# Kernel tuning notes

Hardware: AMD Instinct MI355X
Metric: run time of the kernel (lower is better)

Reference implementation:

```python
import jax, jax.numpy as jnp
import numpy as np

TAU = 0.1
K = 60.0
CHUNK = 64
B = 1024


def setup_inputs() -> dict:
    key = jax.random.key(0)
    k1, k2, k3, k4, k5, k6 = jax.random.split(key, 6)
    s_v = jax.random.normal(k1, (B, B), dtype=jnp.float32)
    s_l = jax.random.normal(k2, (B, B), dtype=jnp.float32)
    pos_mask = jax.random.randint(k3, (B, B), 0, 2).astype(jnp.bool_)
    neg_mask = jax.random.randint(k4, (B, B), 0, 2).astype(jnp.bool_)
    w_v = jax.random.uniform(k5, (B, B), dtype=jnp.float32)
    w_l = jax.random.uniform(k6, (B, B), dtype=jnp.float32)
    return {"s_v": s_v, "s_l": s_l, "pos_mask": pos_mask,
            "neg_mask": neg_mask, "w_v": w_v, "w_l": w_l}


def _soft_ranks(sim, pos_f, neg_f, tau):
    """Chunked differentiable soft ranks. sim/pos_f/neg_f: [B, B] float."""
    b = sim.shape[0]
    n_chunks = b // CHUNK
    sim_c = sim.reshape(n_chunks, CHUNK, b)
    pos_c = pos_f.reshape(n_chunks, CHUNK, b)
    neg_c = neg_f.reshape(n_chunks, CHUNK, b)

    def per_chunk(args):
        cs, pf, nf = args  # each [CHUNK, B]
        # diff[c, a, b] = s[c, a] - s[c, b]
        sig = jax.nn.sigmoid((cs[:, :, None] - cs[:, None, :]) / tau)  # [CHUNK, B, B]
        rank_pos = 1.0 + jnp.einsum('cab,ca->cb', sig, nf)  # count negatives above
        rank_neg = 1.0 + jnp.einsum('cab,ca->cb', sig, pf)  # count positives above
        return rank_pos * pf + rank_neg * nf

    ranks = jax.lax.map(per_chunk, (sim_c, pos_c, neg_c))  # [n_chunks, CHUNK, B]
    return ranks.reshape(b, b)


def reference(s_v, s_l, pos_mask, neg_mask, w_v, w_l):
    pos_f = pos_mask.astype(s_v.dtype)
    neg_f = neg_mask.astype(s_v.dtype)
    rank_v = _soft_ranks(s_v, pos_f, neg_f, TAU)
    rank_l = _soft_ranks(s_l, pos_f, neg_f, TAU)
    S_hat = (K + 1.0) * (w_v / (K + rank_v) + w_l / (K + rank_l))
    return S_hat
```

## Files before the change

kernel.cpp:

```cpp
#include <hip/hip_runtime.h>
#include <hip/hip_fp16.h>

constexpr int B = 1024;
constexpr int NT = 256;
constexpr int NB = 60;
constexpr int SLOTCAP = 1216;
constexpr int QCAP = SLOTCAP / 4;
constexpr int QPHYS = QCAP + (QCAP >> 4) + 1;
constexpr float L2E = 1.4426950408889634f;
constexpr int TCOLS = NB + 6;

constexpr int OFF_EN  = 0;
constexpr int OFF_CQ  = OFF_EN + SLOTCAP * 4;
constexpr int OFF_SEG = OFF_CQ + 2 * QPHYS * 16;
constexpr int OFF_BKQ = OFF_SEG + 14 * TCOLS * 4;
constexpr int OFF_SST = OFF_BKQ + QCAP;
constexpr int OFF_RED = OFF_SST + (NB + 1) * 4;
constexpr int POOL_BYTES = ((OFF_RED + 32 + 15) / 16) * 16;

__global__ __launch_bounds__(NT, 8)
void rank_one_kernel(const float* __restrict__ s_v, const float* __restrict__ s_l,
                     const int* __restrict__ pos_m, const int* __restrict__ neg_m,
                     float* __restrict__ rank_ws) {
    __shared__ __align__(16) char pool[POOL_BYTES];
    float* En          = (float*)(pool + OFF_EN);
    float4* CeAll      = (float4*)(pool + OFF_CQ);
    uint4* ChAll       = (uint4*)(pool + OFF_CQ + QPHYS*16);
    unsigned char (*segCnt)[16]  = (unsigned char(*)[16])(pool + OFF_SEG);
    unsigned short (*segPre)[16] = (unsigned short(*)[16])(pool + OFF_SEG + NB*16);
    float* TabF        = (float*)(pool + OFF_SEG);
    int* segStart      = (int*)(pool + OFF_SST);
    float* Red         = (float*)(pool + OFF_RED);
    float* ANnode      = (float*)(pool + OFF_CQ);
    float* APnode      = ANnode + 64;

    const int m = blockIdx.x >> 10;
    const int r = blockIdx.x & 1023;
    const float* __restrict__ S = m ? s_l : s_v;
    const int tid = threadIdx.x;
    const int lane = tid & 63;
    const int wvid = tid >> 6;
    const unsigned long long lmask = (1ull << lane) - 1ull;

    for (int s = tid; s < SLOTCAP; s += NT) En[s] = 0.f;
    for (int j = tid; j < NB * 16 / 4; j += NT) ((int*)segCnt)[j] = 0;
    __syncthreads();

    float uu[4]; int cat[4];
    float mn = 1e30f, mx = -1e30f;
#pragma unroll
    for (int i = 0; i < 4; ++i) {
        const int c = tid + i * NT;
        uu[i] = S[r * B + c] * 10.0f;
        const int pf = pos_m[r * B + c] != 0, nf = neg_m[r * B + c] != 0;
        cat[i] = pf | (nf << 1);
        mn = fminf(mn, uu[i]); mx = fmaxf(mx, uu[i]);
    }
#pragma unroll
    for (int off = 1; off < 64; off <<= 1) {
        mn = fminf(mn, __shfl_xor(mn, off));
        mx = fmaxf(mx, __shfl_xor(mx, off));
    }
    if (lane == 0) { Red[wvid] = mn; Red[4 + wvid] = mx; }
    __syncthreads();

    const float lo = fminf(fminf(Red[0], Red[1]), fminf(Red[2], Red[3]));
    const float hi = fmaxf(fmaxf(Red[4], Red[5]), fmaxf(Red[6], Red[7]));
    const float umin = lo;
    const float Wb   = fmaxf((hi - lo) * (1.0001f / NB), 1.0f);
    const float invW = 1.0f / Wb;
    const float kap1 = exp2f(-Wb * L2E);
    const float kap2 = kap1 * kap1;
    const float kap3 = kap2 * kap1;
    const float eWm  = exp2f(Wb * L2E);

    int key[4], rk[4];
#pragma unroll
    for (int i = 0; i < 4; ++i) {
        int b = (int)((uu[i] - umin) * invW);
        b = b > NB - 1 ? NB - 1 : b;
        const int kk = cat[i] ? b : 63;
        key[i] = b;
        unsigned long long same = ~0ull;
#pragma unroll
        for (int j = 0; j < 6; ++j) {
            const unsigned long long bb = __ballot((kk >> j) & 1);
            same &= ((kk >> j) & 1) ? bb : ~bb;
        }
        rk[i] = (int)__popcll(same & lmask);
        if (cat[i] && rk[i] == 0)
            segCnt[kk][i * 4 + wvid] = (unsigned char)__popcll(same);
    }
    __syncthreads();

    for (int j = tid; j < NB * 16; j += NT) {
        const int k = j >> 4, u = j & 15;
        int p = 0;
        for (int v = 0; v < u; ++v) p += (int)segCnt[k][v];
        segPre[k][u] = (unsigned short)p;
    }
    if (wvid == 0) {
        int t = 0;
        if (lane < NB) {
#pragma unroll
            for (int u = 0; u < 16; ++u) t += (int)segCnt[lane][u];
            t = (t + 3) & ~3;
        }
        int inc = t;
#pragma unroll
        for (int d = 1; d < 64; d <<= 1) {
            const int o = __shfl_up(inc, d);
            if (lane >= d) inc += o;
        }
        if (lane < NB) segStart[lane] = inc - t;
        if (lane == NB - 1) segStart[NB] = inc;
    }
    __syncthreads();

#pragma unroll
    for (int i = 0; i < 4; ++i) {
        if (cat[i]) {
            const int k = key[i];
            const int slot = segStart[k] + (int)segPre[k][i * 4 + wvid] + rk[i];
            const float cb = umin + ((float)k + 0.5f) * Wb;
            const float env = exp2f((uu[i] - cb) * L2E);
            unsigned eb = __float_as_uint(env);
            eb = (eb & ~3u) | (unsigned)cat[i];
            En[slot] = __uint_as_float(eb);
        }
    }
    __syncthreads();

    const int nS = segStart[NB];
    const int nQ = nS >> 2;

    if (tid < 14 * 6) {
        const int row = tid / 6, ci = tid % 6;
        TabF[row * TCOLS + (ci < 2 ? ci : ci + 60)] = 0.f;
    }
    for (int q = tid; q < nQ; q += NT) {
        const float4 e4v = *(const float4*)&En[4 * q];
        const float en[4] = {e4v.x, e4v.y, e4v.z, e4v.w};
        const int fl[4] = {(int)(__float_as_uint(e4v.x) & 3u),
                           (int)(__float_as_uint(e4v.y) & 3u),
                           (int)(__float_as_uint(e4v.z) & 3u),
                           (int)(__float_as_uint(e4v.w) & 3u)};
        const float s01 = en[0] + en[1], p01 = en[0] * en[1];
        const float s23 = en[2] + en[3], p23 = en[2] * en[3];
        const float e1 = s01 + s23;
        const float e2 = fmaf(s01, s23, p01 + p23);
        const float e3 = fmaf(s01, p23, s23 * p01);
        const float e4 = p01 * p23;
        float nA3 = 0.f, nA2 = 0.f, nA1 = 0.f, nA0 = 0.f;
        float nP3 = 0.f, nP2 = 0.f, nP1 = 0.f, nP0 = 0.f;
#pragma unroll
        for (int j = 0; j < 4; ++j) {
            const float b1 = e1 - en[j];
            const float b2 = fmaf(-en[j], b1, e2);
            const float b3 = fmaf(-en[j], b2, e3);
            const float nn = (float)(fl[j] >> 1) * en[j];
            const float pp = (float)(fl[j] & 1) * en[j];
            nA3 += nn; nA2 = fmaf(nn, b1, nA2); nA1 = fmaf(nn, b2, nA1); nA0 = fmaf(nn, b3, nA0);
            nP3 += pp; nP2 = fmaf(pp, b1, nP2); nP1 = fmaf(pp, b2, nP1); nP0 = fmaf(pp, b3, nP0);
        }
        const int pq = q + (q >> 4);
        CeAll[pq] = make_float4(e1, e2, e3, e4);
        __half2 hA0 = __floats2half2_rn(nA3, nA2);
        __half2 hA1 = __floats2half2_rn(nA1, nA0);
        __half2 hP0 = __floats2half2_rn(nP3, nP2);
        __half2 hP1 = __floats2half2_rn(nP1, nP0);
        ChAll[pq] = make_uint4(reinterpret_cast<unsigned&>(hA0), reinterpret_cast<unsigned&>(hA1),
                               reinterpret_cast<unsigned&>(hP0), reinterpret_cast<unsigned&>(hP1));
    }
    if (tid < NB * 4) {
        const int k = tid >> 2, o = tid & 3;
        float g1a=0,g2a=0,g3a=0,h1a=0,h2a=0,h3a=0,s0a=0;
        float g1p=0,g2p=0,g3p=0,h1p=0,h2p=0,h3p=0,s0p=0;
        for (int s = segStart[k] + o; s < segStart[k + 1]; s += 4) {
            const float en = En[s];
            const int f = (int)(__float_as_uint(en) & 3u);
            if (!f) continue;
            const float en2 = en * en, en3 = en2 * en;
            const float ren = __builtin_amdgcn_rcpf(en);
            const float ren2 = ren * ren, ren3 = ren2 * ren;
            const float nf = (float)(f >> 1), pf = (float)(f & 1);
            g1a = fmaf(nf,en,g1a);  g2a = fmaf(nf,en2,g2a);  g3a = fmaf(nf,en3,g3a);
            h1a = fmaf(nf,ren,h1a); h2a = fmaf(nf,ren2,h2a); h3a = fmaf(nf,ren3,h3a); s0a += nf;
            g1p = fmaf(pf,en,g1p);  g2p = fmaf(pf,en2,g2p);  g3p = fmaf(pf,en3,g3p);
            h1p = fmaf(pf,ren,h1p); h2p = fmaf(pf,ren2,h2p); h3p = fmaf(pf,ren3,h3p); s0p += pf;
        }
#define RED4(v) v += __shfl_xor(v, 2); v += __shfl_xor(v, 1)
        RED4(g1a); RED4(g2a); RED4(g3a); RED4(h1a); RED4(h2a); RED4(h3a); RED4(s0a);
        RED4(g1p); RED4(g2p); RED4(g3p); RED4(h1p); RED4(h2p); RED4(h3p); RED4(s0p);
#undef RED4
        if (o == 0) {
            TabF[(0*7+0)*TCOLS+k+2]=g1a; TabF[(0*7+1)*TCOLS+k+2]=g2a; TabF[(0*7+2)*TCOLS+k+2]=g3a;
            TabF[(0*7+3)*TCOLS+k+2]=h1a; TabF[(0*7+4)*TCOLS+k+2]=h2a; TabF[(0*7+5)*TCOLS+k+2]=h3a;
            TabF[(0*7+6)*TCOLS+k+2]=s0a;
            TabF[(1*7+0)*TCOLS+k+2]=g1p; TabF[(1*7+1)*TCOLS+k+2]=g2p; TabF[(1*7+2)*TCOLS+k+2]=g3p;
            TabF[(1*7+3)*TCOLS+k+2]=h1p; TabF[(1*7+4)*TCOLS+k+2]=h2p; TabF[(1*7+5)*TCOLS+k+2]=h3p;
            TabF[(1*7+6)*TCOLS+k+2]=s0p;
        }
    }
    __syncthreads();
    for (int rowi = wvid; rowi < 14; rowi += 4) {
        const int r7 = rowi % 7;
        float* Trow = &TabF[rowi * TCOLS];
        float v = (lane < NB) ? Trow[lane + 2] : 0.f;
        if (r7 < 3) {
            float kp = (r7 == 0) ? kap1 : (r7 == 1 ? kap2 : kap3);
#pragma unroll
            for (int d = 1; d < 64; d <<= 1) {
                const float o = __shfl_up(v, d);
                if (lane >= d) v = fmaf(kp, o, v);
                kp *= kp;
            }
        } else {
            float kp = (r7 == 3) ? kap1 : (r7 == 4 ? kap2 : (r7 == 5 ? kap3 : 1.0f));
#pragma unroll
            for (int d = 1; d < 64; d <<= 1) {
                float o = __shfl_down(v, d);
                if (lane + d > 63) o = 0.f;
                v = fmaf(kp, o, v);
                kp *= kp;
            }
        }
        if (lane < NB) Trow[lane + 2] = v;
    }
    __syncthreads();

    const int nd = tid >> 2;
    const int no = tid & 3;
    float ANv = 0.f, APv = 0.f;
    if (nd < NB) {
        const int klo = nd > 0 ? nd - 1 : 0;
        const int khi = nd < NB - 1 ? nd + 1 : NB - 1;
        const int qs  = segStart[klo] >> 2;
        const int qe  = segStart[khi + 1] >> 2;
        const int qo0 = segStart[nd] >> 2;
        const int qo1 = segStart[nd + 1] >> 2;
        for (int q = qs + no; q < qe; q += 4) {
            const float x = (q < qo0) ? eWm : ((q >= qo1) ? kap1 : 1.0f);
            const int pq = q + (q >> 4);
            const float4 ce = CeAll[pq];
            const uint4 ch = ChAll[pq];
            const float2 a01 = __half22float2(*(const __half2*)&ch.x);
            const float2 a23 = __half22float2(*(const __half2*)&ch.y);
            const float2 p01 = __half22float2(*(const __half2*)&ch.z);
            const float2 p23 = __half22float2(*(const __half2*)&ch.w);
            float t = x + ce.x; t = fmaf(t, x, ce.y); t = fmaf(t, x, ce.z);
            const float D = fmaf(t, x, ce.w);
            float u = fmaf(a01.x, x, a01.y); u = fmaf(u, x, a23.x);
            const float NA = fmaf(u, x, a23.y);
            float v = fmaf(p01.x, x, p01.y); v = fmaf(v, x, p23.x);
            const float NP = fmaf(v, x, p23.y);
            const float rd = __builtin_amdgcn_rcpf(D);
            ANv = fmaf(NA, rd, ANv);
            APv = fmaf(NP, rd, APv);
        }
        ANv += __shfl_xor(ANv, 2); ANv += __shfl_xor(ANv, 1);
        APv += __shfl_xor(APv, 2); APv += __shfl_xor(APv, 1);
        const float k2 = kap2, k4 = kap2 * kap2, k6 = k4 * kap2;
        ANv += k2 * TabF[(0*7+0)*TCOLS+nd] - k4 * TabF[(0*7+1)*TCOLS+nd] + k6 * TabF[(0*7+2)*TCOLS+nd]
             + TabF[(0*7+6)*TCOLS+nd+4] - k2 * TabF[(0*7+3)*TCOLS+nd+4]
             + k4 * TabF[(0*7+4)*TCOLS+nd+4] - k6 * TabF[(0*7+5)*TCOLS+nd+4];
        APv += k2 * TabF[(1*7+0)*TCOLS+nd] - k4 * TabF[(1*7+1)*TCOLS+nd] + k6 * TabF[(1*7+2)*TCOLS+nd]
             + TabF[(1*7+6)*TCOLS+nd+4] - k2 * TabF[(1*7+3)*TCOLS+nd+4]
             + k4 * TabF[(1*7+4)*TCOLS+nd+4] - k6 * TabF[(1*7+5)*TCOLS+nd+4];
    }
    __syncthreads();
    if (nd < NB && no == 0) { ANnode[nd] = ANv; APnode[nd] = APv; }
    __syncthreads();

#pragma unroll
    for (int i = 0; i < 4; ++i) {
        const float t = (uu[i] - umin) * invW - 0.5f;
        int jc = (int)floorf(t);
        jc = jc < 1 ? 1 : (jc > NB - 3 ? NB - 3 : jc);
        const float s = t - (float)jc;
        const float sm = s - 1.f, sp = s + 1.f, s2 = s - 2.f;
        const float wL = -s * sm * s2 * (1.f / 6.f);
        const float w0 = sp * sm * s2 * 0.5f;
        const float w1 = -sp * s * s2 * 0.5f;
        const float w2 = sp * s * sm * (1.f / 6.f);
        const float AN = wL * ANnode[jc-1] + w0 * ANnode[jc] + w1 * ANnode[jc+1] + w2 * ANnode[jc+2];
        const float AP = wL * APnode[jc-1] + w0 * APnode[jc] + w1 * APnode[jc+1] + w2 * APnode[jc+2];
        const bool pf = (cat[i] & 1) != 0;
        const bool nf = (cat[i] & 2) != 0;
        const float rk_ = (pf ? 1.f + AN : 0.f) + (nf ? 1.f + AP : 0.f);
        rank_ws[m * (B * B) + r * B + (tid + i * NT)] = rk_;
    }
}

__global__ __launch_bounds__(NT, 8)
void combine_kernel(const float* __restrict__ rank_ws,
                    const float* __restrict__ w_v, const float* __restrict__ w_l,
                    float* __restrict__ out) {
    const int i4 = (blockIdx.x * NT + threadIdx.x) * 4;
    const float4 rv = *(const float4*)&rank_ws[i4];
    const float4 rl = *(const float4*)&rank_ws[B * B + i4];
    const float4 wv = *(const float4*)&w_v[i4];
    const float4 wl = *(const float4*)&w_l[i4];
    float4 o;
    o.x = 61.f * (wv.x / (60.f + rv.x) + wl.x / (60.f + rl.x));
    o.y = 61.f * (wv.y / (60.f + rv.y) + wl.y / (60.f + rl.y));
    o.z = 61.f * (wv.z / (60.f + rv.z) + wl.z / (60.f + rl.z));
    o.w = 61.f * (wv.w / (60.f + rv.w) + wl.w / (60.f + rl.w));
    *(float4*)&out[i4] = o;
}

extern "C" void kernel_launch(void* const* d_in, const int* in_sizes, int n_in,
                              void* d_out, int out_size, void* d_ws, size_t ws_size,
                              hipStream_t stream) {
    const float* s_v = (const float*)d_in[0];
    const float* s_l = (const float*)d_in[1];
    const int* pos_mask = (const int*)d_in[2];
    const int* neg_mask = (const int*)d_in[3];
    const float* w_v = (const float*)d_in[4];
    const float* w_l = (const float*)d_in[5];
    float* out = (float*)d_out;
    float* rank_ws = (float*)d_ws;

    rank_one_kernel<<<2 * B, NT, 0, stream>>>(s_v, s_l, pos_mask, neg_mask, rank_ws);
    combine_kernel<<<(B * B) / (NT * 4), NT, 0, stream>>>(rank_ws, w_v, w_l, out);
}
```

Before: 31.21 us.

## Fuse both modality rank computations and combine step into one kernel per row

Each block now processes one row for both s_v and s_l in sequence, reusing the mask loads and shared-memory scratch, and writes the final combined output directly. This removes the 8 MB rank workspace round trip through global memory and the second kernel launch. In exchange the grid halves to 1024 blocks, each running the two passes serially, which reduces the parallelism available to hide latency.

```diff
diff --git a/kernel.cpp b/kernel.cpp
--- a/kernel.cpp
+++ b/kernel.cpp
@@ -13,15 +13,15 @@
 constexpr int OFF_EN  = 0;
 constexpr int OFF_CQ  = OFF_EN + SLOTCAP * 4;
 constexpr int OFF_SEG = OFF_CQ + 2 * QPHYS * 16;
-constexpr int OFF_BKQ = OFF_SEG + 14 * TCOLS * 4;
-constexpr int OFF_SST = OFF_BKQ + QCAP;
+constexpr int OFF_SST = OFF_SEG + 14 * TCOLS * 4;
 constexpr int OFF_RED = OFF_SST + (NB + 1) * 4;
-constexpr int POOL_BYTES = ((OFF_RED + 32 + 15) / 16) * 16;
+constexpr int POOL_BYTES = ((OFF_RED + 64 + 15) / 16) * 16;
 
 __global__ __launch_bounds__(NT, 8)
-void rank_one_kernel(const float* __restrict__ s_v, const float* __restrict__ s_l,
-                     const int* __restrict__ pos_m, const int* __restrict__ neg_m,
-                     float* __restrict__ rank_ws) {
+void rank_fused_kernel(const float* __restrict__ s_v, const float* __restrict__ s_l,
+                       const int* __restrict__ pos_m, const int* __restrict__ neg_m,
+                       const float* __restrict__ w_v, const float* __restrict__ w_l,
+                       float* __restrict__ out) {
     __shared__ __align__(16) char pool[POOL_BYTES];
     float* En          = (float*)(pool + OFF_EN);
     float4* CeAll      = (float4*)(pool + OFF_CQ);
@@ -34,279 +34,285 @@
     float* ANnode      = (float*)(pool + OFF_CQ);
     float* APnode      = ANnode + 64;
 
-    const int m = blockIdx.x >> 10;
-    const int r = blockIdx.x & 1023;
-    const float* __restrict__ S = m ? s_l : s_v;
+    const int r = blockIdx.x;
     const int tid = threadIdx.x;
     const int lane = tid & 63;
     const int wvid = tid >> 6;
     const unsigned long long lmask = (1ull << lane) - 1ull;
 
-    for (int s = tid; s < SLOTCAP; s += NT) En[s] = 0.f;
-    for (int j = tid; j < NB * 16 / 4; j += NT) ((int*)segCnt)[j] = 0;
-    __syncthreads();
-
-    float uu[4]; int cat[4];
-    float mn = 1e30f, mx = -1e30f;
+    float uu[2][4]; int cat[4];
+    float mn0 = 1e30f, mx0 = -1e30f, mn1 = 1e30f, mx1 = -1e30f;
 #pragma unroll
     for (int i = 0; i < 4; ++i) {
         const int c = tid + i * NT;
-        uu[i] = S[r * B + c] * 10.0f;
+        uu[0][i] = s_v[r * B + c] * 10.0f;
+        uu[1][i] = s_l[r * B + c] * 10.0f;
         const int pf = pos_m[r * B + c] != 0, nf = neg_m[r * B + c] != 0;
         cat[i] = pf | (nf << 1);
-        mn = fminf(mn, uu[i]); mx = fmaxf(mx, uu[i]);
+        mn0 = fminf(mn0, uu[0][i]); mx0 = fmaxf(mx0, uu[0][i]);
+        mn1 = fminf(mn1, uu[1][i]); mx1 = fmaxf(mx1, uu[1][i]);
     }
 #pragma unroll
     for (int off = 1; off < 64; off <<= 1) {
-        mn = fminf(mn, __shfl_xor(mn, off));
-        mx = fmaxf(mx, __shfl_xor(mx, off));
-    }
-    if (lane == 0) { Red[wvid] = mn; Red[4 + wvid] = mx; }
+        mn0 = fminf(mn0, __shfl_xor(mn0, off)); mx0 = fmaxf(mx0, __shfl_xor(mx0, off));
+        mn1 = fminf(mn1, __shfl_xor(mn1, off)); mx1 = fmaxf(mx1, __shfl_xor(mx1, off));
+    }
+    if (lane == 0) {
+        Red[0 + wvid] = mn0; Red[4 + wvid] = mx0;
+        Red[8 + wvid] = mn1; Red[12 + wvid] = mx1;
+    }
     __syncthreads();
 
-    const float lo = fminf(fminf(Red[0], Red[1]), fminf(Red[2], Red[3]));
-    const float hi = fmaxf(fmaxf(Red[4], Red[5]), fmaxf(Red[6], Red[7]));
-    const float umin = lo;
-    const float Wb   = fmaxf((hi - lo) * (1.0001f / NB), 1.0f);
-    const float invW = 1.0f / Wb;
-    const float kap1 = exp2f(-Wb * L2E);
-    const float kap2 = kap1 * kap1;
-    const float kap3 = kap2 * kap1;
-    const float eWm  = exp2f(Wb * L2E);
-
-    int key[4], rk[4];
+    float umin2[2], Wb2[2], invW2[2], kapA[2], kapB[2], kapC[2], eWm2[2];
+#pragma unroll
+    for (int mp = 0; mp < 2; ++mp) {
+        const float lo = fminf(fminf(Red[8*mp+0], Red[8*mp+1]), fminf(Red[8*mp+2], Red[8*mp+3]));
+        const float hi = fmaxf(fmaxf(Red[8*mp+4], Red[8*mp+5]), fmaxf(Red[8*mp+6], Red[8*mp+7]));
+        umin2[mp] = lo;
+        Wb2[mp]   = fmaxf((hi - lo) * (1.0001f / NB), 1.0f);
+        invW2[mp] = 1.0f / Wb2[mp];
+        kapA[mp]  = exp2f(-Wb2[mp] * L2E);
+        kapB[mp]  = kapA[mp] * kapA[mp];
+        kapC[mp]  = kapB[mp] * kapA[mp];
+        eWm2[mp]  = exp2f(Wb2[mp] * L2E);
+    }
+
+    float rkm[2][4];
+
+#pragma unroll
+    for (int mp = 0; mp < 2; ++mp) {
+        const float umin = umin2[mp], Wb = Wb2[mp], invW = invW2[mp];
+        const float kap1 = kapA[mp], kap2 = kapB[mp], kap3 = kapC[mp], eWm = eWm2[mp];
+
+        __syncthreads();
+        for (int s = tid; s < SLOTCAP; s += NT) En[s] = 0.f;
+        for (int j = tid; j < NB * 16 / 4; j += NT) ((int*)segCnt)[j] = 0;
+        __syncthreads();
+
+        int key[4], rk[4];
+#pragma unroll
+        for (int i = 0; i < 4; ++i) {
+            int b = (int)((uu[mp][i] - umin) * invW);
+            b = b > NB - 1 ? NB - 1 : b;
+            const int kk = cat[i] ? b : 63;
+            key[i] = b;
+            unsigned long long same = ~0ull;
+#pragma unroll
+            for (int j = 0; j < 6; ++j) {
+                const unsigned long long bb = __ballot((kk >> j) & 1);
+                same &= ((kk >> j) & 1) ? bb : ~bb;
+            }
+            rk[i] = (int)__popcll(same & lmask);
+            if (cat[i] && rk[i] == 0)
+                segCnt[kk][i * 4 + wvid] = (unsigned char)__popcll(same);
+        }
+        __syncthreads();
+
+        for (int j = tid; j < NB * 16; j += NT) {
+            const int k = j >> 4, u = j & 15;
+            int p = 0;
+            for (int v = 0; v < u; ++v) p += (int)segCnt[k][v];
+            segPre[k][u] = (unsigned short)p;
+        }
+        if (wvid == 0) {
+            int t = 0;
+            if (lane < NB) {
+#pragma unroll
+                for (int u = 0; u < 16; ++u) t += (int)segCnt[lane][u];
+                t = (t + 3) & ~3;
+            }
+            int inc = t;
+#pragma unroll
+            for (int d = 1; d < 64; d <<= 1) {
+                const int o = __shfl_up(inc, d);
+                if (lane >= d) inc += o;
+            }
+            if (lane < NB) segStart[lane] = inc - t;
+            if (lane == NB - 1) segStart[NB] = inc;
+        }
+        __syncthreads();
+
+#pragma unroll
+        for (int i = 0; i < 4; ++i) {
+            if (cat[i]) {
+                const int k = key[i];
+                const int slot = segStart[k] + (int)segPre[k][i * 4 + wvid] + rk[i];
+                const float cb = umin + ((float)k + 0.5f) * Wb;
+                const float env = exp2f((uu[mp][i] - cb) * L2E);
+                unsigned eb = __float_as_uint(env);
+                eb = (eb & ~3u) | (unsigned)cat[i];
+                En[slot] = __uint_as_float(eb);
+            }
+        }
+        __syncthreads();
+
+        const int nS = segStart[NB];
+        const int nQ = nS >> 2;
+
+        if (tid < 14 * 6) {
+            const int row = tid / 6, ci = tid % 6;
+            TabF[row * TCOLS + (ci < 2 ? ci : ci + 60)] = 0.f;
+        }
+        for (int q = tid; q < nQ; q += NT) {
+            const float4 e4v = *(const float4*)&En[4 * q];
+            const float en[4] = {e4v.x, e4v.y, e4v.z, e4v.w};
+            const int fl[4] = {(int)(__float_as_uint(e4v.x) & 3u),
+                               (int)(__float_as_uint(e4v.y) & 3u),
+                               (int)(__float_as_uint(e4v.z) & 3u),
+                               (int)(__float_as_uint(e4v.w) & 3u)};
+            const float s01 = en[0] + en[1], p01 = en[0] * en[1];
+            const float s23 = en[2] + en[3], p23 = en[2] * en[3];
+            const float e1 = s01 + s23;
+            const float e2 = fmaf(s01, s23, p01 + p23);
+            const float e3 = fmaf(s01, p23, s23 * p01);
+            const float e4 = p01 * p23;
+            float nA3 = 0.f, nA2 = 0.f, nA1 = 0.f, nA0 = 0.f;
+            float nP3 = 0.f, nP2 = 0.f, nP1 = 0.f, nP0 = 0.f;
+#pragma unroll
+            for (int j = 0; j < 4; ++j) {
+                const float b1 = e1 - en[j];
+                const float b2 = fmaf(-en[j], b1, e2);
+                const float b3 = fmaf(-en[j], b2, e3);
+                const float nn = (float)(fl[j] >> 1) * en[j];
+                const float pp = (float)(fl[j] & 1) * en[j];
+                nA3 += nn; nA2 = fmaf(nn, b1, nA2); nA1 = fmaf(nn, b2, nA1); nA0 = fmaf(nn, b3, nA0);
+                nP3 += pp; nP2 = fmaf(pp, b1, nP2); nP1 = fmaf(pp, b2, nP1); nP0 = fmaf(pp, b3, nP0);
+            }
+            const int pq = q + (q >> 4);
+            CeAll[pq] = make_float4(e1, e2, e3, e4);
+            __half2 hA0 = __floats2half2_rn(nA3, nA2);
+            __half2 hA1 = __floats2half2_rn(nA1, nA0);
+            __half2 hP0 = __floats2half2_rn(nP3, nP2);
+            __half2 hP1 = __floats2half2_rn(nP1, nP0);
+            ChAll[pq] = make_uint4(reinterpret_cast<unsigned&>(hA0), reinterpret_cast<unsigned&>(hA1),
+                                   reinterpret_cast<unsigned&>(hP0), reinterpret_cast<unsigned&>(hP1));
+        }
+        if (tid < NB * 4) {
+            const int k = tid >> 2, o = tid & 3;
+            float g1a=0,g2a=0,g3a=0,h1a=0,h2a=0,h3a=0,s0a=0;
+            float g1p=0,g2p=0,g3p=0,h1p=0,h2p=0,h3p=0,s0p=0;
+            for (int s = segStart[k] + o; s < segStart[k + 1]; s += 4) {
+                const float en = En[s];
+                const int f = (int)(__float_as_uint(en) & 3u);
+                if (!f) continue;
+                const float en2 = en * en, en3 = en2 * en;
+                const float ren = __builtin_amdgcn_rcpf(en);
+                const float ren2 = ren * ren, ren3 = ren2 * ren;
+                const float nf = (float)(f >> 1), pf = (float)(f & 1);
+                g1a = fmaf(nf,en,g1a);  g2a = fmaf(nf,en2,g2a);  g3a = fmaf(nf,en3,g3a);
+                h1a = fmaf(nf,ren,h1a); h2a = fmaf(nf,ren2,h2a); h3a = fmaf(nf,ren3,h3a); s0a += nf;
+                g1p = fmaf(pf,en,g1p);  g2p = fmaf(pf,en2,g2p);  g3p = fmaf(pf,en3,g3p);
+                h1p = fmaf(pf,ren,h1p); h2p = fmaf(pf,ren2,h2p); h3p = fmaf(pf,ren3,h3p); s0p += pf;
+            }
+#define RED4(v) v += __shfl_xor(v, 2); v += __shfl_xor(v, 1)
+            RED4(g1a); RED4(g2a); RED4(g3a); RED4(h1a); RED4(h2a); RED4(h3a); RED4(s0a);
+            RED4(g1p); RED4(g2p); RED4(g3p); RED4(h1p); RED4(h2p); RED4(h3p); RED4(s0p);
+#undef RED4
+            if (o == 0) {
+                TabF[(0*7+0)*TCOLS+k+2]=g1a; TabF[(0*7+1)*TCOLS+k+2]=g2a; TabF[(0*7+2)*TCOLS+k+2]=g3a;
+                TabF[(0*7+3)*TCOLS+k+2]=h1a; TabF[(0*7+4)*TCOLS+k+2]=h2a; TabF[(0*7+5)*TCOLS+k+2]=h3a;
+                TabF[(0*7+6)*TCOLS+k+2]=s0a;
+                TabF[(1*7+0)*TCOLS+k+2]=g1p; TabF[(1*7+1)*TCOLS+k+2]=g2p; TabF[(1*7+2)*TCOLS+k+2]=g3p;
+                TabF[(1*7+3)*TCOLS+k+2]=h1p; TabF[(1*7+4)*TCOLS+k+2]=h2p; TabF[(1*7+5)*TCOLS+k+2]=h3p;
+                TabF[(1*7+6)*TCOLS+k+2]=s0p;
+            }
+        }
+        __syncthreads();
+        for (int rowi = wvid; rowi < 14; rowi += 4) {
+            const int r7 = rowi % 7;
+            float* Trow = &TabF[rowi * TCOLS];
+            float v = (lane < NB) ? Trow[lane + 2] : 0.f;
+            if (r7 < 3) {
+                float kp = (r7 == 0) ? kap1 : (r7 == 1 ? kap2 : kap3);
+#pragma unroll
+                for (int d = 1; d < 64; d <<= 1) {
+                    const float o = __shfl_up(v, d);
+                    if (lane >= d) v = fmaf(kp, o, v);
+                    kp *= kp;
+                }
+            } else {
+                float kp = (r7 == 3) ? kap1 : (r7 == 4 ? kap2 : (r7 == 5 ? kap3 : 1.0f));
+#pragma unroll
+                for (int d = 1; d < 64; d <<= 1) {
+                    float o = __shfl_down(v, d);
+                    if (lane + d > 63) o = 0.f;
+                    v = fmaf(kp, o, v);
+                    kp *= kp;
+                }
+            }
+            if (lane < NB) Trow[lane + 2] = v;
+        }
+        __syncthreads();
+
+        const int nd = tid >> 2;
+        const int no = tid & 3;
+        float ANv = 0.f, APv = 0.f;
+        if (nd < NB) {
+            const int klo = nd > 0 ? nd - 1 : 0;
+            const int khi = nd < NB - 1 ? nd + 1 : NB - 1;
+            const int qs  = segStart[klo] >> 2;
+            const int qe  = segStart[khi + 1] >> 2;
+            const int qo0 = segStart[nd] >> 2;
+            const int qo1 = segStart[nd + 1] >> 2;
+            for (int q = qs + no; q < qe; q += 4) {
+                const float x = (q < qo0) ? eWm : ((q >= qo1) ? kap1 : 1.0f);
+                const int pq = q + (q >> 4);
+                const float4 ce = CeAll[pq];
+                const uint4 ch = ChAll[pq];
+                const float2 a01 = __half22float2(*(const __half2*)&ch.x);
+                const float2 a23 = __half22float2(*(const __half2*)&ch.y);
+                const float2 p01 = __half22float2(*(const __half2*)&ch.z);
+                const float2 p23 = __half22float2(*(const __half2*)&ch.w);
+                float t = x + ce.x; t = fmaf(t, x, ce.y); t = fmaf(t, x, ce.z);
+                const float D = fmaf(t, x, ce.w);
+                float u = fmaf(a01.x, x, a01.y); u = fmaf(u, x, a23.x);
+                const float NA = fmaf(u, x, a23.y);
+                float v = fmaf(p01.x, x, p01.y); v = fmaf(v, x, p23.x);
+                const float NP = fmaf(v, x, p23.y);
+                const float rd = __builtin_amdgcn_rcpf(D);
+                ANv = fmaf(NA, rd, ANv);
+                APv = fmaf(NP, rd, APv);
+            }
+            ANv += __shfl_xor(ANv, 2); ANv += __shfl_xor(ANv, 1);
+            APv += __shfl_xor(APv, 2); APv += __shfl_xor(APv, 1);
+            const float k2 = kap2, k4 = kap2 * kap2, k6 = k4 * kap2;
+            ANv += k2 * TabF[(0*7+0)*TCOLS+nd] - k4 * TabF[(0*7+1)*TCOLS+nd] + k6 * TabF[(0*7+2)*TCOLS+nd]
+                 + TabF[(0*7+6)*TCOLS+nd+4] - k2 * TabF[(0*7+3)*TCOLS+nd+4]
+                 + k4 * TabF[(0*7+4)*TCOLS+nd+4] - k6 * TabF[(0*7+5)*TCOLS+nd+4];
+            APv += k2 * TabF[(1*7+0)*TCOLS+nd] - k4 * TabF[(1*7+1)*TCOLS+nd] + k6 * TabF[(1*7+2)*TCOLS+nd]
+                 + TabF[(1*7+6)*TCOLS+nd+4] - k2 * TabF[(1*7+3)*TCOLS+nd+4]
+                 + k4 * TabF[(1*7+4)*TCOLS+nd+4] - k6 * TabF[(1*7+5)*TCOLS+nd+4];
+        }
+        __syncthreads();
+        if (nd < NB && no == 0) { ANnode[nd] = ANv; APnode[nd] = APv; }
+        __syncthreads();
+
+#pragma unroll
+        for (int i = 0; i < 4; ++i) {
+            const float t = (uu[mp][i] - umin) * invW - 0.5f;
+            int jc = (int)floorf(t);
+            jc = jc < 1 ? 1 : (jc > NB - 3 ? NB - 3 : jc);
+            const float s = t - (float)jc;
+            const float sm = s - 1.f, sp = s + 1.f, s2 = s - 2.f;
+            const float wL = -s * sm * s2 * (1.f / 6.f);
+            const float w0 = sp * sm * s2 * 0.5f;
+            const float w1 = -sp * s * s2 * 0.5f;
+            const float w2 = sp * s * sm * (1.f / 6.f);
+            const float AN = wL * ANnode[jc-1] + w0 * ANnode[jc] + w1 * ANnode[jc+1] + w2 * ANnode[jc+2];
+            const float AP = wL * APnode[jc-1] + w0 * APnode[jc] + w1 * APnode[jc+1] + w2 * APnode[jc+2];
+            const bool pf = (cat[i] & 1) != 0;
+            const bool nf = (cat[i] & 2) != 0;
+            rkm[mp][i] = (pf ? 1.f + AN : 0.f) + (nf ? 1.f + AP : 0.f);
+        }
+    }
+
 #pragma unroll
     for (int i = 0; i < 4; ++i) {
-        int b = (int)((uu[i] - umin) * invW);
-        b = b > NB - 1 ? NB - 1 : b;
-        const int kk = cat[i] ? b : 63;
-        key[i] = b;
-        unsigned long long same = ~0ull;
-#pragma unroll
-        for (int j = 0; j < 6; ++j) {
-            const unsigned long long bb = __ballot((kk >> j) & 1);
-            same &= ((kk >> j) & 1) ? bb : ~bb;
-        }
-        rk[i] = (int)__popcll(same & lmask);
-        if (cat[i] && rk[i] == 0)
-            segCnt[kk][i * 4 + wvid] = (unsigned char)__popcll(same);
-    }
-    __syncthreads();
-
-    for (int j = tid; j < NB * 16; j += NT) {
-        const int k = j >> 4, u = j & 15;
-        int p = 0;
-        for (int v = 0; v < u; ++v) p += (int)segCnt[k][v];
-        segPre[k][u] = (unsigned short)p;
-    }
-    if (wvid == 0) {
-        int t = 0;
-        if (lane < NB) {
-#pragma unroll
-            for (int u = 0; u < 16; ++u) t += (int)segCnt[lane][u];
-            t = (t + 3) & ~3;
-        }
-        int inc = t;
-#pragma unroll
-        for (int d = 1; d < 64; d <<= 1) {
-            const int o = __shfl_up(inc, d);
-            if (lane >= d) inc += o;
-        }
-        if (lane < NB) segStart[lane] = inc - t;
-        if (lane == NB - 1) segStart[NB] = inc;
-    }
-    __syncthreads();
-
-#pragma unroll
-    for (int i = 0; i < 4; ++i) {
-        if (cat[i]) {
-            const int k = key[i];
-            const int slot = segStart[k] + (int)segPre[k][i * 4 + wvid] + rk[i];
-            const float cb = umin + ((float)k + 0.5f) * Wb;
-            const float env = exp2f((uu[i] - cb) * L2E);
-            unsigned eb = __float_as_uint(env);
-            eb = (eb & ~3u) | (unsigned)cat[i];
-            En[slot] = __uint_as_float(eb);
-        }
-    }
-    __syncthreads();
-
-    const int nS = segStart[NB];
-    const int nQ = nS >> 2;
-
-    if (tid < 14 * 6) {
-        const int row = tid / 6, ci = tid % 6;
-        TabF[row * TCOLS + (ci < 2 ? ci : ci + 60)] = 0.f;
-    }
-    for (int q = tid; q < nQ; q += NT) {
-        const float4 e4v = *(const float4*)&En[4 * q];
-        const float en[4] = {e4v.x, e4v.y, e4v.z, e4v.w};
-        const int fl[4] = {(int)(__float_as_uint(e4v.x) & 3u),
-                           (int)(__float_as_uint(e4v.y) & 3u),
-                           (int)(__float_as_uint(e4v.z) & 3u),
-                           (int)(__float_as_uint(e4v.w) & 3u)};
-        const float s01 = en[0] + en[1], p01 = en[0] * en[1];
-        const float s23 = en[2] + en[3], p23 = en[2] * en[3];
-        const float e1 = s01 + s23;
-        const float e2 = fmaf(s01, s23, p01 + p23);
-        const float e3 = fmaf(s01, p23, s23 * p01);
-        const float e4 = p01 * p23;
-        float nA3 = 0.f, nA2 = 0.f, nA1 = 0.f, nA0 = 0.f;
-        float nP3 = 0.f, nP2 = 0.f, nP1 = 0.f, nP0 = 0.f;
-#pragma unroll
-        for (int j = 0; j < 4; ++j) {
-            const float b1 = e1 - en[j];
-            const float b2 = fmaf(-en[j], b1, e2);
-            const float b3 = fmaf(-en[j], b2, e3);
-            const float nn = (float)(fl[j] >> 1) * en[j];
-            const float pp = (float)(fl[j] & 1) * en[j];
-            nA3 += nn; nA2 = fmaf(nn, b1, nA2); nA1 = fmaf(nn, b2, nA1); nA0 = fmaf(nn, b3, nA0);
-            nP3 += pp; nP2 = fmaf(pp, b1, nP2); nP1 = fmaf(pp, b2, nP1); nP0 = fmaf(pp, b3, nP0);
-        }
-        const int pq = q + (q >> 4);
-        CeAll[pq] = make_float4(e1, e2, e3, e4);
-        __half2 hA0 = __floats2half2_rn(nA3, nA2);
-        __half2 hA1 = __floats2half2_rn(nA1, nA0);
-        __half2 hP0 = __floats2half2_rn(nP3, nP2);
-        __half2 hP1 = __floats2half2_rn(nP1, nP0);
-        ChAll[pq] = make_uint4(reinterpret_cast<unsigned&>(hA0), reinterpret_cast<unsigned&>(hA1),
-                               reinterpret_cast<unsigned&>(hP0), reinterpret_cast<unsigned&>(hP1));
-    }
-    if (tid < NB * 4) {
-        const int k = tid >> 2, o = tid & 3;
-        float g1a=0,g2a=0,g3a=0,h1a=0,h2a=0,h3a=0,s0a=0;
-        float g1p=0,g2p=0,g3p=0,h1p=0,h2p=0,h3p=0,s0p=0;
-        for (int s = segStart[k] + o; s < segStart[k + 1]; s += 4) {
-            const float en = En[s];
-            const int f = (int)(__float_as_uint(en) & 3u);
-            if (!f) continue;
-            const float en2 = en * en, en3 = en2 * en;
-            const float ren = __builtin_amdgcn_rcpf(en);
-            const float ren2 = ren * ren, ren3 = ren2 * ren;
-            const float nf = (float)(f >> 1), pf = (float)(f & 1);
-            g1a = fmaf(nf,en,g1a);  g2a = fmaf(nf,en2,g2a);  g3a = fmaf(nf,en3,g3a);
-            h1a = fmaf(nf,ren,h1a); h2a = fmaf(nf,ren2,h2a); h3a = fmaf(nf,ren3,h3a); s0a += nf;
-            g1p = fmaf(pf,en,g1p);  g2p = fmaf(pf,en2,g2p);  g3p = fmaf(pf,en3,g3p);
-            h1p = fmaf(pf,ren,h1p); h2p = fmaf(pf,ren2,h2p); h3p = fmaf(pf,ren3,h3p); s0p += pf;
-        }
-#define RED4(v) v += __shfl_xor(v, 2); v += __shfl_xor(v, 1)
-        RED4(g1a); RED4(g2a); RED4(g3a); RED4(h1a); RED4(h2a); RED4(h3a); RED4(s0a);
-        RED4(g1p); RED4(g2p); RED4(g3p); RED4(h1p); RED4(h2p); RED4(h3p); RED4(s0p);
-#undef RED4
-        if (o == 0) {
-            TabF[(0*7+0)*TCOLS+k+2]=g1a; TabF[(0*7+1)*TCOLS+k+2]=g2a; TabF[(0*7+2)*TCOLS+k+2]=g3a;
-            TabF[(0*7+3)*TCOLS+k+2]=h1a; TabF[(0*7+4)*TCOLS+k+2]=h2a; TabF[(0*7+5)*TCOLS+k+2]=h3a;
-            TabF[(0*7+6)*TCOLS+k+2]=s0a;
-            TabF[(1*7+0)*TCOLS+k+2]=g1p; TabF[(1*7+1)*TCOLS+k+2]=g2p; TabF[(1*7+2)*TCOLS+k+2]=g3p;
-            TabF[(1*7+3)*TCOLS+k+2]=h1p; TabF[(1*7+4)*TCOLS+k+2]=h2p; TabF[(1*7+5)*TCOLS+k+2]=h3p;
-            TabF[(1*7+6)*TCOLS+k+2]=s0p;
-        }
-    }
-    __syncthreads();
-    for (int rowi = wvid; rowi < 14; rowi += 4) {
-        const int r7 = rowi % 7;
-        float* Trow = &TabF[rowi * TCOLS];
-        float v = (lane < NB) ? Trow[lane + 2] : 0.f;
-        if (r7 < 3) {
-            float kp = (r7 == 0) ? kap1 : (r7 == 1 ? kap2 : kap3);
-#pragma unroll
-            for (int d = 1; d < 64; d <<= 1) {
-                const float o = __shfl_up(v, d);
-                if (lane >= d) v = fmaf(kp, o, v);
-                kp *= kp;
-            }
-        } else {
-            float kp = (r7 == 3) ? kap1 : (r7 == 4 ? kap2 : (r7 == 5 ? kap3 : 1.0f));
-#pragma unroll
-            for (int d = 1; d < 64; d <<= 1) {
-                float o = __shfl_down(v, d);
-                if (lane + d > 63) o = 0.f;
-                v = fmaf(kp, o, v);
-                kp *= kp;
-            }
-        }
-        if (lane < NB) Trow[lane + 2] = v;
-    }
-    __syncthreads();
-
-    const int nd = tid >> 2;
-    const int no = tid & 3;
-    float ANv = 0.f, APv = 0.f;
-    if (nd < NB) {
-        const int klo = nd > 0 ? nd - 1 : 0;
-        const int khi = nd < NB - 1 ? nd + 1 : NB - 1;
-        const int qs  = segStart[klo] >> 2;
-        const int qe  = segStart[khi + 1] >> 2;
-        const int qo0 = segStart[nd] >> 2;
-        const int qo1 = segStart[nd + 1] >> 2;
-        for (int q = qs + no; q < qe; q += 4) {
-            const float x = (q < qo0) ? eWm : ((q >= qo1) ? kap1 : 1.0f);
-            const int pq = q + (q >> 4);
-            const float4 ce = CeAll[pq];
-            const uint4 ch = ChAll[pq];
-            const float2 a01 = __half22float2(*(const __half2*)&ch.x);
-            const float2 a23 = __half22float2(*(const __half2*)&ch.y);
-            const float2 p01 = __half22float2(*(const __half2*)&ch.z);
-            const float2 p23 = __half22float2(*(const __half2*)&ch.w);
-            float t = x + ce.x; t = fmaf(t, x, ce.y); t = fmaf(t, x, ce.z);
-            const float D = fmaf(t, x, ce.w);
-            float u = fmaf(a01.x, x, a01.y); u = fmaf(u, x, a23.x);
-            const float NA = fmaf(u, x, a23.y);
-            float v = fmaf(p01.x, x, p01.y); v = fmaf(v, x, p23.x);
-            const float NP = fmaf(v, x, p23.y);
-            const float rd = __builtin_amdgcn_rcpf(D);
-            ANv = fmaf(NA, rd, ANv);
-            APv = fmaf(NP, rd, APv);
-        }
-        ANv += __shfl_xor(ANv, 2); ANv += __shfl_xor(ANv, 1);
-        APv += __shfl_xor(APv, 2); APv += __shfl_xor(APv, 1);
-        const float k2 = kap2, k4 = kap2 * kap2, k6 = k4 * kap2;
-        ANv += k2 * TabF[(0*7+0)*TCOLS+nd] - k4 * TabF[(0*7+1)*TCOLS+nd] + k6 * TabF[(0*7+2)*TCOLS+nd]
-             + TabF[(0*7+6)*TCOLS+nd+4] - k2 * TabF[(0*7+3)*TCOLS+nd+4]
-             + k4 * TabF[(0*7+4)*TCOLS+nd+4] - k6 * TabF[(0*7+5)*TCOLS+nd+4];
-        APv += k2 * TabF[(1*7+0)*TCOLS+nd] - k4 * TabF[(1*7+1)*TCOLS+nd] + k6 * TabF[(1*7+2)*TCOLS+nd]
-             + TabF[(1*7+6)*TCOLS+nd+4] - k2 * TabF[(1*7+3)*TCOLS+nd+4]
-             + k4 * TabF[(1*7+4)*TCOLS+nd+4] - k6 * TabF[(1*7+5)*TCOLS+nd+4];
-    }
-    __syncthreads();
-    if (nd < NB && no == 0) { ANnode[nd] = ANv; APnode[nd] = APv; }
-    __syncthreads();
-
-#pragma unroll
-    for (int i = 0; i < 4; ++i) {
-        const float t = (uu[i] - umin) * invW - 0.5f;
-        int jc = (int)floorf(t);
-        jc = jc < 1 ? 1 : (jc > NB - 3 ? NB - 3 : jc);
-        const float s = t - (float)jc;
-        const float sm = s - 1.f, sp = s + 1.f, s2 = s - 2.f;
-        const float wL = -s * sm * s2 * (1.f / 6.f);
-        const float w0 = sp * sm * s2 * 0.5f;
-        const float w1 = -sp * s * s2 * 0.5f;
-        const float w2 = sp * s * sm * (1.f / 6.f);
-        const float AN = wL * ANnode[jc-1] + w0 * ANnode[jc] + w1 * ANnode[jc+1] + w2 * ANnode[jc+2];
-        const float AP = wL * APnode[jc-1] + w0 * APnode[jc] + w1 * APnode[jc+1] + w2 * APnode[jc+2];
-        const bool pf = (cat[i] & 1) != 0;
-        const bool nf = (cat[i] & 2) != 0;
-        const float rk_ = (pf ? 1.f + AN : 0.f) + (nf ? 1.f + AP : 0.f);
-        rank_ws[m * (B * B) + r * B + (tid + i * NT)] = rk_;
-    }
-}
-
-__global__ __launch_bounds__(NT, 8)
-void combine_kernel(const float* __restrict__ rank_ws,
-                    const float* __restrict__ w_v, const float* __restrict__ w_l,
-                    float* __restrict__ out) {
-    const int i4 = (blockIdx.x * NT + threadIdx.x) * 4;
-    const float4 rv = *(const float4*)&rank_ws[i4];
-    const float4 rl = *(const float4*)&rank_ws[B * B + i4];
-    const float4 wv = *(const float4*)&w_v[i4];
-    const float4 wl = *(const float4*)&w_l[i4];
-    float4 o;
-    o.x = 61.f * (wv.x / (60.f + rv.x) + wl.x / (60.f + rl.x));
-    o.y = 61.f * (wv.y / (60.f + rv.y) + wl.y / (60.f + rl.y));
-    o.z = 61.f * (wv.z / (60.f + rv.z) + wl.z / (60.f + rl.z));
-    o.w = 61.f * (wv.w / (60.f + rv.w) + wl.w / (60.f + rl.w));
-    *(float4*)&out[i4] = o;
+        const int c = tid + i * NT;
+        const float wv = w_v[r * B + c];
+        const float wl = w_l[r * B + c];
+        out[r * B + c] = 61.f * (wv / (60.f + rkm[0][i]) + wl / (60.f + rkm[1][i]));
+    }
 }
 
 extern "C" void kernel_launch(void* const* d_in, const int* in_sizes, int n_in,
@@ -319,8 +325,7 @@
     const float* w_v = (const float*)d_in[4];
     const float* w_l = (const float*)d_in[5];
     float* out = (float*)d_out;
-    float* rank_ws = (float*)d_ws;
-
-    rank_one_kernel<<<2 * B, NT, 0, stream>>>(s_v, s_l, pos_mask, neg_mask, rank_ws);
-    combine_kernel<<<(B * B) / (NT * 4), NT, 0, stream>>>(rank_ws, w_v, w_l, out);
+
+    rank_fused_kernel<<<B, NT, 0, stream>>>(s_v, s_l, pos_mask, neg_mask,
+                                            w_v, w_l, out);
 }
```

New measurement: 40.99 us. +31.3%, slower.
